# Performance work log

Measured on AMD Instinct MI355X. Metric: run time of the kernel, lower is better.

## Reference

```python
import jax, jax.numpy as jnp
import numpy as np

N = 500
HG = 16
D = 512
STEPS = 16


def _gcn_norm(edge_index, n):
    # PyG GCNConv: add self-loops, symmetric normalization
    src = jnp.concatenate([edge_index[0], jnp.arange(n)])
    dst = jnp.concatenate([edge_index[1], jnp.arange(n)])
    deg = jax.ops.segment_sum(jnp.ones_like(dst, dtype=jnp.float32), dst, num_segments=n)
    dinv = jnp.where(deg > 0, jax.lax.rsqrt(jnp.maximum(deg, 1.0)), 0.0)
    norm = dinv[src] * dinv[dst]
    return src, dst, norm


def _gcn(h, src, dst, norm, W, b):
    # h: (B, N, F) -> (B, N, HG);  out_i = sum_{j->i} norm_ji * (h_j W) + b
    hW = h @ W                              # (B, N, HG)
    t = jnp.swapaxes(hW, 0, 1)              # (N, B, HG)
    msg = t[src] * norm[:, None, None]      # (E', B, HG)
    agg = jax.ops.segment_sum(msg, dst, num_segments=h.shape[1])
    return jnp.swapaxes(agg, 0, 1) + b


def _gru_step(h, xt, Wih, Whh, bih, bhh):
    gi = xt @ Wih.T + bih                    # (B, 3D)
    gh = h @ Whh.T + bhh
    ir, iz, inn = jnp.split(gi, 3, axis=-1)
    hr, hz, hn = jnp.split(gh, 3, axis=-1)
    r = jax.nn.sigmoid(ir + hr)
    z = jax.nn.sigmoid(iz + hz)
    n = jnp.tanh(inn + r * hn)
    return (1.0 - z) * n + z * h


def setup_inputs() -> dict:
    key = jax.random.key(0)
    ks = jax.random.split(key, 16)
    B, T, F = 32, 64, 8
    E = 16000
    s = lambda fan_in: 1.0 / np.sqrt(fan_in)
    u = lambda k, shape, sc: jax.random.uniform(k, shape, jnp.float32, -sc, sc)
    return {
        "x": jax.random.normal(ks[0], (B, T, N, F), jnp.float32),
        "decoder_initial_input": jax.random.normal(ks[1], (B, N, 1), jnp.float32),
        "edge_index": jax.random.randint(ks[2], (2, E), 0, N),
        "gcn_enc_W": u(ks[3], (F, HG), s(F)),
        "gcn_enc_b": jnp.zeros((HG,), jnp.float32),
        "gcn_dec_W": u(ks[4], (1, HG), 1.0),
        "gcn_dec_b": jnp.zeros((HG,), jnp.float32),
        "enc_Wih": u(ks[5], (3 * D, N * HG), s(D)),
        "enc_Whh": u(ks[6], (3 * D, D), s(D)),
        "enc_bih": u(ks[7], (3 * D,), s(D)),
        "enc_bhh": u(ks[8], (3 * D,), s(D)),
        "dec_Wih": u(ks[9], (3 * D, N * HG), s(D)),
        "dec_Whh": u(ks[10], (3 * D, D), s(D)),
        "dec_bih": u(ks[11], (3 * D,), s(D)),
        "dec_bhh": u(ks[12], (3 * D,), s(D)),
        "fc_W": u(ks[13], (N, D), s(D)),
        "fc_b": u(ks[14], (N,), s(D)),
    }


def reference(x, decoder_initial_input, edge_index,
              gcn_enc_W, gcn_enc_b, gcn_dec_W, gcn_dec_b,
              enc_Wih, enc_Whh, enc_bih, enc_bhh,
              dec_Wih, dec_Whh, dec_bih, dec_bhh,
              fc_W, fc_b):
    B, T, n, F = x.shape
    src, dst, norm = _gcn_norm(edge_index, n)

    # ---- encoder: GCN over all (B,T) at once, then GRU scan over T ----
    emb = jax.nn.relu(_gcn(x.reshape(B * T, n, F), src, dst, norm, gcn_enc_W, gcn_enc_b))
    flat = emb.reshape(B, T, n * HG)
    xs = jnp.swapaxes(flat, 0, 1)            # (T, B, N*HG)
    h0 = jnp.zeros((B, D), jnp.float32)

    def enc_body(h, xt):
        return _gru_step(h, xt, enc_Wih, enc_Whh, enc_bih, enc_bhh), None

    hidden, _ = jax.lax.scan(enc_body, h0, xs)

    def dec_body(carry, _):
        h, inp = carry                        # inp: (B, N, 1)
        e = jax.nn.relu(_gcn(inp, src, dst, norm, gcn_dec_W, gcn_dec_b))
        h = _gru_step(h, e.reshape(B, n * HG), dec_Wih, dec_Whh, dec_bih, dec_bhh)
        out = h @ fc_W.T + fc_b               # (B, N)
        return (h, out[:, :, None]), out

    (_, _), outs = jax.lax.scan(dec_body, (hidden, decoder_initial_input), None, length=STEPS)
    return jnp.swapaxes(outs, 0, 1)           # (B, STEPS, N)
```

## Files before the change

### kernel.cpp

```cpp
#include <hip/hip_runtime.h>
#include <stdint.h>

typedef short short8 __attribute__((ext_vector_type(8)));
typedef float f32x4 __attribute__((ext_vector_type(4)));
typedef float f32x16 __attribute__((ext_vector_type(16)));

#define N_NODES 500
#define HGC 16
#define DH 512
#define T_STEPS 64
#define NB 32
#define F_IN 8
#define DSTEPS 16
#define E_EDGES 16000
#define E_TOT 16500
#define NH 8000
#define G3 1536
#define BT 2048
#define DKC 10
#define DNT 48
#define DBLK 480

__device__ __forceinline__ unsigned short f2bf(float x) {
  unsigned int u = __float_as_uint(x);
  u = (u + 0x7fffu + ((u >> 16) & 1u)) >> 16;
  return (unsigned short)u;
}

__device__ __forceinline__ void gl_lds16(const void* g, void* l) {
  __builtin_amdgcn_global_load_lds((const __attribute__((address_space(1))) void*)g,
                                   (__attribute__((address_space(3))) void*)l, 16, 0, 0);
}

__device__ __forceinline__ float sigm(float x) { return 1.f / (1.f + __expf(-x)); }

__global__ __launch_bounds__(512) void k_graph(const int* __restrict__ ei,
                                               int* __restrict__ rowptr,
                                               int* __restrict__ colg, float* __restrict__ nrmg) {
  __shared__ int degL[512];
  __shared__ int scanL[512];
  __shared__ int curL[512];
  __shared__ float dinvL[512];
  int t = threadIdx.x;
  degL[t] = (t < N_NODES) ? 1 : 0;
  __syncthreads();
  for (int e = t; e < E_EDGES; e += 512) atomicAdd(&degL[ei[E_EDGES + e]], 1);
  __syncthreads();
  int v = degL[t];
  scanL[t] = v;
  __syncthreads();
  for (int off = 1; off < 512; off <<= 1) {
    int add = (t >= off) ? scanL[t - off] : 0;
    __syncthreads();
    scanL[t] += add;
    __syncthreads();
  }
  int excl = scanL[t] - v;
  if (t < N_NODES) {
    rowptr[t] = excl;
    curL[t] = excl;
    dinvL[t] = rsqrtf((float)v);
  }
  if (t == 0) rowptr[N_NODES] = scanL[511];
  __syncthreads();
  for (int e = t; e < E_TOT; e += 512) {
    int s_, d_;
    if (e < E_EDGES) { s_ = ei[e]; d_ = ei[E_EDGES + e]; }
    else { s_ = d_ = e - E_EDGES; }
    int pos = atomicAdd(&curL[d_], 1);
    colg[pos] = s_;
    nrmg[pos] = dinvL[s_] * dinvL[d_];
  }
}

__global__ void k_f2bf_all(const float* __restrict__ a, unsigned short* __restrict__ da, int n4a,
                           const float* __restrict__ b, unsigned short* __restrict__ db, int n4b,
                           const float* __restrict__ c, unsigned short* __restrict__ dc, int n4c) {
  int i = blockIdx.x * blockDim.x + threadIdx.x;
  const float* s;
  unsigned short* d;
  int j = i;
  if (j < n4a) { s = a; d = da; }
  else {
    j -= n4a;
    if (j < n4b) { s = b; d = db; }
    else {
      j -= n4b;
      if (j >= n4c) return;
      s = c; d = dc;
    }
  }
  float4 v = ((const float4*)s)[j];
  ushort4 o;
  o.x = f2bf(v.x); o.y = f2bf(v.y); o.z = f2bf(v.z); o.w = f2bf(v.w);
  ((ushort4*)d)[j] = o;
}

__global__ void k_f2bf_fc(const float* __restrict__ fcW, unsigned short* __restrict__ fcWb) {
  int i = blockIdx.x * 256 + threadIdx.x;
  if (i >= 512 * 512 / 4) return;
  int row = i >> 7;
  ushort4 o = {0, 0, 0, 0};
  if (row < N_NODES) {
    float4 v = ((const float4*)fcW)[i];
    o.x = f2bf(v.x); o.y = f2bf(v.y); o.z = f2bf(v.z); o.w = f2bf(v.w);
  }
  ((ushort4*)fcWb)[i] = o;
}

__global__ __launch_bounds__(256) void k_repack(const float* __restrict__ dWih,
                                                unsigned short* __restrict__ wihDp) {
  int i = blockIdx.x * 256 + threadIdx.x;
  if (i >= DBLK * 50 * 32) return;
  int blob = i / 1600, r = i - blob * 1600;
  int nd = r >> 5, col = r & 31;
  int ntile = blob / DKC, kc = blob - ntile * DKC;
  const float* src = dWih + (size_t)(ntile * 32 + col) * NH + kc * 800 + nd * 16;
  short8 lo, hi;
#pragma unroll
  for (int c = 0; c < 8; ++c) {
    lo[c] = (short)f2bf(src[c]);
    hi[c] = (short)f2bf(src[c + 8]);
  }
  unsigned short* dst = wihDp + (size_t)blob * 25600 + nd * 512 + col * 8;
  *(short8*)dst = lo;
  *(short8*)(dst + 256) = hi;
}

__global__ __launch_bounds__(256) void k_transpose(const float* __restrict__ x,
                                                   unsigned short* __restrict__ xT2) {
  __shared__ float xs[N_NODES * 9];
  int g = blockIdx.x, t = threadIdx.x;
  const float4* xg = (const float4*)(x + (size_t)g * (N_NODES * F_IN));
  for (int i = t; i < N_NODES * 2; i += 256) {
    float4 v = xg[i];
    int n = i >> 1, fh = (i & 1) * 4;
    float* d = &xs[n * 9 + fh];
    d[0] = v.x; d[1] = v.y; d[2] = v.z; d[3] = v.w;
  }
  __syncthreads();
  int f = t >> 5, u = t & 31;
  short8 lo, hi;
#pragma unroll
  for (int j = 0; j < 8; ++j) {
    int n0 = u * 16 + j, n1 = n0 + 8;
    lo[j] = (short)((n0 < N_NODES) ? f2bf(xs[n0 * 9 + f]) : 0);
    hi[j] = (short)((n1 < N_NODES) ? f2bf(xs[n1 * 9 + f]) : 0);
  }
  unsigned short* dst = xT2 + (size_t)(g * 8 + f) * 512 + u * 16;
  *(short8*)dst = lo;
  *(short8*)(dst + 8) = hi;
}

__global__ __launch_bounds__(256) void k_densify(const int* __restrict__ rowptr,
                                                 const int* __restrict__ col,
                                                 const float* __restrict__ nrm,
                                                 unsigned short* __restrict__ AhatD) {
  __shared__ float row[512];
  int n = blockIdx.x, t = threadIdx.x;
  row[t] = 0.f; row[t + 256] = 0.f;
  __syncthreads();
  if (n < N_NODES) {
    int e1 = rowptr[n + 1];
    for (int e = rowptr[n] + t; e < e1; e += 256) atomicAdd(&row[col[e]], nrm[e]);
  }
  __syncthreads();
  AhatD[n * 512 + t] = f2bf(row[t]);
  AhatD[n * 512 + t + 256] = f2bf(row[t + 256]);
}

__global__ __launch_bounds__(256) void k_gemm_agg(const unsigned short* __restrict__ A,
                                                  const unsigned short* __restrict__ B,
                                                  const float* __restrict__ W,
                                                  const float* __restrict__ bias,
                                                  unsigned short* __restrict__ emb) {
  __shared__ float smem[64 * 129];
  __shared__ float Wsm[F_IN * HGC];
  __shared__ float bsm[HGC];
  unsigned short* As = (unsigned short*)smem;
  unsigned short* Bs = As + 4096;
  int t = threadIdx.x;
  if (t < F_IN * HGC) Wsm[t] = W[t];
  if (t < HGC) bsm[t] = bias[t];
  int m0 = blockIdx.x * 128, n0 = blockIdx.y * 128;
  int wave = t >> 6, lane = t & 63;
  int mh = (wave >> 1) * 64, nh = (wave & 1) * 64;
  int lrow = t >> 2, lslot = t & 3;
  f32x4 acc[4][4];
#pragma unroll
  for (int a = 0; a < 4; ++a)
#pragma unroll
    for (int b = 0; b < 4; ++b) acc[a][b] = (f32x4){0.f, 0.f, 0.f, 0.f};
  const unsigned short* ga0 = A + (size_t)(m0 + lrow) * 512 + lslot * 8;
  const unsigned short* ga1 = A + (size_t)(m0 + 64 + lrow) * 512 + lslot * 8;
  const unsigned short* gb0 = B + (size_t)(n0 + lrow) * 512 + lslot * 8;
  const unsigned short* gb1 = B + (size_t)(n0 + 64 + lrow) * 512 + lslot * 8;
  int rl = lane & 15, ks = lane >> 4;
  for (int kt = 0; kt < 16; ++kt) {
    int k0 = kt * 32;
    gl_lds16(ga0 + k0, &As[t * 8]);
    gl_lds16(ga1 + k0, &As[2048 + t * 8]);
    gl_lds16(gb0 + k0, &Bs[t * 8]);
    gl_lds16(gb1 + k0, &Bs[2048 + t * 8]);
    __syncthreads();
    short8 af[4], bfr[4];
#pragma unroll
    for (int mf = 0; mf < 4; ++mf) af[mf] = *(const short8*)&As[(mh + mf * 16 + rl) * 32 + ks * 8];
#pragma unroll
    for (int nf = 0; nf < 4; ++nf) bfr[nf] = *(const short8*)&Bs[(nh + nf * 16 + rl) * 32 + ks * 8];
#pragma unroll
    for (int mf = 0; mf < 4; ++mf)
#pragma unroll
      for (int nf = 0; nf < 4; ++nf)
        acc[mf][nf] = __builtin_amdgcn_mfma_f32_16x16x32_bf16(af[mf], bfr[nf], acc[mf][nf], 0, 0, 0);
    __syncthreads();
  }
  int rg = lane >> 4;
  for (int p = 0; p < 2; ++p) {
    if ((wave >> 1) == p) {
#pragma unroll
      for (int mf = 0; mf < 4; ++mf)
#pragma unroll
        for (int nf = 0; nf < 4; ++nf)
#pragma unroll
          for (int q = 0; q < 4; ++q)
            smem[(mf * 16 + rg * 4 + q) * 129 + nh + nf * 16 + rl] = acc[mf][nf][q];
    }
    __syncthreads();
    int gl = t >> 5, sub = t & 31;
    int g = blockIdx.x * 16 + p * 8 + gl;
#pragma unroll
    for (int j = 0; j < 4; ++j) {
      int nl = sub + 32 * j, ng = n0 + nl;
      if (ng < N_NODES) {
        float v[8];
#pragma unroll
        for (int f = 0; f < 8; ++f) v[f] = smem[(gl * 8 + f) * 129 + nl];
        short8 o0, o1;
#pragma unroll
        for (int c = 0; c < 8; ++c) {
          float s0 = bsm[c], s1 = bsm[c + 8];
#pragma unroll
          for (int f = 0; f < 8; ++f) {
            s0 += v[f] * Wsm[f * 16 + c];
            s1 += v[f] * Wsm[f * 16 + c + 8];
          }
          o0[c] = (short)f2bf(fmaxf(s0, 0.f));
          o1[c] = (short)f2bf(fmaxf(s1, 0.f));
        }
        unsigned short* dst = emb + (size_t)g * NH + ng * 16;
        *(short8*)dst = o0;
        *(short8*)(dst + 8) = o1;
      }
    }
    __syncthreads();
  }
}

__global__ __launch_bounds__(256) void k_gemm_enc(
    const unsigned short* __restrict__ A, const unsigned short* __restrict__ Bm,
    float* __restrict__ giP2) {
  __shared__ unsigned short As[128 * 32];
  __shared__ unsigned short Bs[64 * 32];
  int t = threadIdx.x;
  int m0 = blockIdx.x * 128, n0 = blockIdx.y * 64;
  int wave = t >> 6, lane = t & 63;
  int mh = (wave >> 1) * 64, nh = (wave & 1) * 32;
  int lrow = t >> 2, lslot = t & 3;
  f32x4 acc[4][2];
#pragma unroll
  for (int a = 0; a < 4; ++a)
#pragma unroll
    for (int b = 0; b < 2; ++b) acc[a][b] = (f32x4){0.f, 0.f, 0.f, 0.f};
  const unsigned short* ga0 = A + (size_t)(m0 + lrow) * NH + lslot * 8;
  const unsigned short* ga1 = A + (size_t)(m0 + 64 + lrow) * NH + lslot * 8;
  const unsigned short* gb0 = Bm + (size_t)(n0 + lrow) * NH + lslot * 8;
  int rl = lane & 15, ks = lane >> 4;
  for (int kt = 0; kt < 250; ++kt) {
    int k0 = kt * 32;
    gl_lds16(ga0 + k0, &As[t * 8]);
    gl_lds16(ga1 + k0, &As[2048 + t * 8]);
    gl_lds16(gb0 + k0, &Bs[t * 8]);
    __syncthreads();
    short8 af[4], bfr[2];
#pragma unroll
    for (int mf = 0; mf < 4; ++mf) af[mf] = *(const short8*)&As[(mh + mf * 16 + rl) * 32 + ks * 8];
#pragma unroll
    for (int nf = 0; nf < 2; ++nf) bfr[nf] = *(const short8*)&Bs[(nh + nf * 16 + rl) * 32 + ks * 8];
#pragma unroll
    for (int mf = 0; mf < 4; ++mf)
#pragma unroll
      for (int nf = 0; nf < 2; ++nf)
        acc[mf][nf] = __builtin_amdgcn_mfma_f32_16x16x32_bf16(af[mf], bfr[nf], acc[mf][nf], 0, 0, 0);
    __syncthreads();
  }
  int rg = lane >> 4;
  int gate = n0 >> 9;
#pragma unroll
  for (int mf = 0; mf < 4; ++mf)
#pragma unroll
    for (int nf = 0; nf < 2; ++nf) {
      int n = n0 + nh + nf * 16 + rl;
      int d = n & 511, blk = d >> 5, cc = d & 31;
#pragma unroll
      for (int q = 0; q < 4; ++q) {
        int m = m0 + mh + mf * 16 + rg * 4 + q;
        int s = m & 63, bb = m >> 6;
        giP2[(size_t)(s * 16 + blk) * 3072 + gate * 1024 + bb * 32 + cc] = acc[mf][nf][q];
      }
    }
}

__device__ __forceinline__ void stage_hb(const unsigned short* __restrict__ src,
                                         unsigned short* hb, int t) {
  int bw = t >> 3, i8 = t & 7;
  short8 v[8];
#pragma unroll
  for (int i = 0; i < 8; ++i)
    v[i] = *(const short8*)((const char*)src + bw * 1024 + i8 * 128 + i * 16);
#pragma unroll
  for (int i = 0; i < 8; ++i) {
    int kb = i8 * 128 + i * 16;
    *(short8*)((char*)hb + bw * 1024 + (kb ^ ((bw & 15) << 4))) = v[i];
  }
}

__device__ __forceinline__ void gru_core_g(const unsigned short* __restrict__ whhB,
                                           const unsigned short* hb, float* gh,
                                           int t, int c0) {
  int lane = t & 63, g = t >> 6;
  int b31 = lane & 31, kg = lane >> 5;
  if (g < 3) {
    f32x16 acc;
#pragma unroll
    for (int q = 0; q < 16; ++q) acc[q] = 0.f;
    const unsigned short* brow = whhB + (size_t)(g * 512 + c0 + b31) * 512 + kg * 8;
    int asw = (b31 & 15) << 4;
#pragma unroll 4
    for (int kk = 0; kk < 32; ++kk) {
      int kb = (kk * 32 + kg * 16) ^ asw;
      short8 a = *(const short8*)((const char*)hb + b31 * 1024 + kb);
      short8 b = *(const short8*)(brow + kk * 16);
      acc = __builtin_amdgcn_mfma_f32_32x32x16_bf16(a, b, acc, 0, 0, 0);
    }
#pragma unroll
    for (int q = 0; q < 16; ++q) {
      int br = (q & 3) + 8 * (q >> 2) + 4 * kg;
      gh[g * 1024 + br * 32 + b31] = acc[q];
    }
  }
}

__device__ __forceinline__ void gru_gates(const float* gi, const float* gh,
                                          const float* __restrict__ bih,
                                          const float* __restrict__ bhh,
                                          float* __restrict__ hF,
                                          unsigned short* __restrict__ hb_out,
                                          int t, int c0) {
  for (int i = t; i < 1024; i += 256) {
    int b = i >> 5, cc = i & 31, d = c0 + cc;
    float gr = gi[i] + bih[d];
    float gz = gi[1024 + i] + bih[512 + d];
    float gn = gi[2048 + i] + bih[1024 + d];
    float hr = gh[b * 32 + cc] + bhh[d];
    float hz = gh[1024 + b * 32 + cc] + bhh[512 + d];
    float hn = gh[2048 + b * 32 + cc] + bhh[1024 + d];
    float r = sigm(gr + hr), z = sigm(gz + hz);
    float nn = tanhf(gn + r * hn);
    float hp = hF[b * 512 + d];
    float hnew = (1.f - z) * nn + z * hp;
    hF[b * 512 + d] = hnew;
    hb_out[b * 512 + d] = f2bf(hnew);
  }
}

__global__ __launch_bounds__(256, 1) void k_enc_scan(
    const unsigned short* __restrict__ whhB, const float* __restrict__ giP2,
    const float* __restrict__ bih, const float* __restrict__ bhh,
    float* __restrict__ hF, unsigned short* __restrict__ hbA,
    unsigned short* __restrict__ hbB, int* __restrict__ arr) {
  __shared__ unsigned short hb[32 * 512];
  __shared__ float gh[3 * 1024];
  __shared__ float h32[1024];
  __shared__ float gi_lds[3072];
  int t = threadIdx.x, bid = blockIdx.x;
  int c0 = bid * 32;
  int lane = t & 63, g = t >> 6;
  int b31 = lane & 31, kg = lane >> 5;

  short8 wreg[32];
  if (g < 3) {
    const unsigned short* brow = whhB + (size_t)(g * 512 + c0 + b31) * 512 + kg * 8;
#pragma unroll
    for (int kk = 0; kk < 32; ++kk) wreg[kk] = *(const short8*)(brow + kk * 16);
  }
  for (int i = t; i < 1024; i += 256) h32[i] = 0.f;
  int cc = t & 31, d = c0 + cc;
  float bi_r = bih[d], bi_z = bih[512 + d], bi_n = bih[1024 + d];
  float bh_r = bhh[d], bh_z = bhh[512 + d], bh_n = bhh[1024 + d];
  int asw = (b31 & 15) << 4;
  {
    const float* src0 = giP2 + (size_t)bid * 3072;
#pragma unroll
    for (int i = 0; i < 3; ++i)
      gl_lds16(src0 + i * 1024 + t * 4, &gi_lds[i * 1024 + t * 4]);
  }
  __syncthreads();

  for (int s = 0; s < T_STEPS; ++s) {
    const unsigned short* hbin = (s & 1) ? hbB : hbA;
    unsigned short* hbout = (s & 1) ? hbA : hbB;
    if (s > 0 && t < 64) {
      for (;;) {
        int v = __hip_atomic_load(&arr[t & 15], __ATOMIC_ACQUIRE, __HIP_MEMORY_SCOPE_AGENT);
        if (__all(v >= s)) break;
        __builtin_amdgcn_s_sleep(1);
      }
    }
    __syncthreads();
    stage_hb(hbin, hb, t);
    __syncthreads();
    if (g < 3) {
      f32x16 acc0, acc1;
#pragma unroll
      for (int q = 0; q < 16; ++q) { acc0[q] = 0.f; acc1[q] = 0.f; }
      const char* abase = (const char*)hb + b31 * 1024;
#pragma unroll
      for (int kk = 0; kk < 32; ++kk) {
        int kb = (kk * 32 + kg * 16) ^ asw;
        short8 a = *(const short8*)(abase + kb);
        if (kk & 1) acc1 = __builtin_amdgcn_mfma_f32_32x32x16_bf16(a, wreg[kk], acc1, 0, 0, 0);
        else acc0 = __builtin_amdgcn_mfma_f32_32x32x16_bf16(a, wreg[kk], acc0, 0, 0, 0);
      }
#pragma unroll
      for (int q = 0; q < 16; ++q) {
        int br = (q & 3) + 8 * (q >> 2) + 4 * kg;
        gh[g * 1024 + br * 32 + b31] = acc0[q] + acc1[q];
      }
    }
    __syncthreads();
#pragma unroll
    for (int j = 0; j < 4; ++j) {
      int i = t + 256 * j;
      int b = (t >> 5) + 8 * j;
      float r = sigm(gi_lds[i] + bi_r + gh[i] + bh_r);
      float z = sigm(gi_lds[1024 + i] + bi_z + gh[1024 + i] + bh_z);
      float nn = tanhf(gi_lds[2048 + i] + bi_n + r * (gh[2048 + i] + bh_n));
      float hnew = (1.f - z) * nn + z * h32[i];
      h32[i] = hnew;
      hbout[b * 512 + d] = f2bf(hnew);
    }
    __syncthreads();
    if (g == 3 && s + 1 < T_STEPS) {
      const float* srcn = giP2 + (size_t)((s + 1) * 16 + bid) * 3072;
#pragma unroll
      for (int i = 0; i < 12; ++i)
        gl_lds16(srcn + (i * 64 + lane) * 4, &gi_lds[(i * 64 + lane) * 4]);
    }
    if (t == 0) {
      __threadfence();
      __hip_atomic_store(&arr[bid], s + 1, __ATOMIC_RELEASE, __HIP_MEMORY_SCOPE_AGENT);
    }
  }
#pragma unroll
  for (int j = 0; j < 4; ++j) {
    int i = t + 256 * j;
    int b = (t >> 5) + 8 * j;
    hF[b * 512 + d] = h32[i];
  }
}

__global__ __launch_bounds__(64) void k_dec_gemm(
    const unsigned short* __restrict__ wihDp, const unsigned short* __restrict__ E8,
    float* __restrict__ parts) {
  __shared__ unsigned short wlds[25600];
  int bid = blockIdx.x, t = threadIdx.x;
  int b31 = t & 31, kg = t >> 5;
  int ntile = bid / DKC, kc = bid - ntile * DKC;
  const unsigned short* src = wihDp + (size_t)bid * 25600;
#pragma unroll 10
  for (int i = 0; i < 50; ++i)
    gl_lds16(src + i * 512 + t * 8, (char*)wlds + i * 1024 + t * 16);
  __syncthreads();
  f32x16 acc0, acc1;
#pragma unroll
  for (int q = 0; q < 16; ++q) { acc0[q] = 0.f; acc1[q] = 0.f; }
  const unsigned short* ea = E8 + (size_t)b31 * NH + kc * 800 + kg * 8;
  const char* wb = (const char*)wlds + kg * 512 + b31 * 16;
#pragma unroll 5
  for (int nd = 0; nd < 50; nd += 2) {
    short8 a0 = *(const short8*)(ea + nd * 16);
    short8 b0 = *(const short8*)(wb + (size_t)nd * 1024);
    short8 a1 = *(const short8*)(ea + (nd + 1) * 16);
    short8 b1 = *(const short8*)(wb + (size_t)(nd + 1) * 1024);
    acc0 = __builtin_amdgcn_mfma_f32_32x32x16_bf16(a0, b0, acc0, 0, 0, 0);
    acc1 = __builtin_amdgcn_mfma_f32_32x32x16_bf16(a1, b1, acc1, 0, 0, 0);
  }
  float* pp = parts + (size_t)(kc * DNT + ntile) * 1024 + b31;
#pragma unroll
  for (int q = 0; q < 16; ++q) {
    int br = (q & 3) + 8 * (q >> 2) + 4 * kg;
    pp[br * 32] = acc0[q] + acc1[q];
  }
}

__global__ __launch_bounds__(256, 1) void k_gru_fc(
    const unsigned short* __restrict__ whhB, const float* __restrict__ parts,
    const float* __restrict__ bih, const float* __restrict__ bhh,
    float* __restrict__ hF, const unsigned short* __restrict__ hb_in,
    unsigned short* __restrict__ hb_out,
    const unsigned short* __restrict__ fcWb, const float* __restrict__ fcb,
    const float* __restrict__ Wd, const float* __restrict__ bd,
    const int* __restrict__ rowptr, const int* __restrict__ colA, const float* __restrict__ nrmA,
    float* __restrict__ out, unsigned short* __restrict__ E8,
    int* __restrict__ fGRU, int s) {
  __shared__ unsigned short hb[32 * 512];
  __shared__ float gh[3 * 1024];
  __shared__ float gi[3 * 1024];
  int t = threadIdx.x, bid = blockIdx.x;
  int c0 = bid * 32;
  int lane = t & 63, g = t >> 6;
  int b31 = lane & 31, kg = lane >> 5;
  stage_hb(hb_in, hb, t);
  for (int i = t; i < 3072; i += 256) {
    int gg = i >> 10, r = i & 1023, bb = r >> 5, cc2 = r & 31;
    float a = 0.f;
#pragma unroll
    for (int kc = 0; kc < DKC; ++kc)
      a += parts[((size_t)kc * DNT + gg * 16 + bid) * 1024 + bb * 32 + cc2];
    gi[i] = a;
  }
  __syncthreads();
  gru_core_g(whhB, hb, gh, t, c0);
  __syncthreads();
  gru_gates(gi, gh, bih, bhh, hF, hb_out, t, c0);
  __syncthreads();
  if (t == 0) {
    __threadfence();
    __hip_atomic_store(&fGRU[bid], 2 * s + 1, __ATOMIC_RELEASE, __HIP_MEMORY_SCOPE_AGENT);
  }
  if (t < 64) {
    for (;;) {
      int f = __hip_atomic_load(&fGRU[t & 15], __ATOMIC_ACQUIRE, __HIP_MEMORY_SCOPE_AGENT);
      if (__all(f >= 2 * s + 1)) break;
      __builtin_amdgcn_s_sleep(1);
    }
  }
  __syncthreads();
  stage_hb(hb_out, hb, t);
  __syncthreads();
  if (g == 0) {
    f32x16 acc;
#pragma unroll
    for (int q = 0; q < 16; ++q) acc[q] = 0.f;
    int n0 = bid * 32;
    int nrow = n0 + b31;
    const unsigned short* brow = fcWb + (size_t)nrow * 512 + kg * 8;
    const char* abase = (const char*)hb + b31 * 1024;
    int asw = (b31 & 15) << 4;
#pragma unroll 4
    for (int kk = 0; kk < 32; ++kk) {
      int kb = (kk * 32 + kg * 16) ^ asw;
      short8 a = *(const short8*)(abase + kb);
      short8 b = *(const short8*)(brow + kk * 16);
      acc = __builtin_amdgcn_mfma_f32_32x32x16_bf16(a, b, acc, 0, 0, 0);
    }
    if (nrow < N_NODES) {
      float fb = fcb[nrow];
#pragma unroll
      for (int q = 0; q < 16; ++q) {
        int br = (q & 3) + 8 * (q >> 2) + 4 * kg;
        out[(size_t)br * (DSTEPS * N_NODES) + s * N_NODES + nrow] = acc[q] + fb;
      }
    }
  }
  __syncthreads();
  if (t == 0) {
    __threadfence();
    __hip_atomic_store(&fGRU[bid], 2 * s + 2, __ATOMIC_RELEASE, __HIP_MEMORY_SCOPE_AGENT);
  }
  if (t < 64) {
    for (;;) {
      int f = __hip_atomic_load(&fGRU[t & 15], __ATOMIC_ACQUIRE, __HIP_MEMORY_SCOPE_AGENT);
      if (__all(f >= 2 * s + 2)) break;
      __builtin_amdgcn_s_sleep(1);
    }
  }
  __syncthreads();
  float* orow = gi;
  float* wds = gh;
  float* bds = gh + 16;
  int b0 = bid * 2;
  for (int i = t; i < 1000; i += 256) {
    int bb = (i >= 500) ? 1 : 0;
    int n = i - bb * 500;
    orow[bb * 512 + n] = out[(size_t)(b0 + bb) * (DSTEPS * N_NODES) + s * N_NODES + n];
  }
  if (t < HGC) { wds[t] = Wd[t]; bds[t] = bd[t]; }
  __syncthreads();
  for (int n = t; n < N_NODES; n += 256) {
    int e1 = rowptr[n + 1];
    float a0 = 0.f, a1 = 0.f;
    for (int e = rowptr[n]; e < e1; ++e) {
      int c = colA[e];
      float wv = nrmA[e];
      a0 += wv * orow[c];
      a1 += wv * orow[512 + c];
    }
    short8 l0, h0v, l1, h1v;
#pragma unroll
    for (int c = 0; c < 8; ++c) {
      l0[c] = (short)f2bf(fmaxf(a0 * wds[c] + bds[c], 0.f));
      h0v[c] = (short)f2bf(fmaxf(a0 * wds[c + 8] + bds[c + 8], 0.f));
      l1[c] = (short)f2bf(fmaxf(a1 * wds[c] + bds[c], 0.f));
      h1v[c] = (short)f2bf(fmaxf(a1 * wds[c + 8] + bds[c + 8], 0.f));
    }
    unsigned short* d0 = E8 + (size_t)b0 * NH + n * 16;
    unsigned short* d1 = E8 + (size_t)(b0 + 1) * NH + n * 16;
    *(short8*)d0 = l0;
    *(short8*)(d0 + 8) = h0v;
    *(short8*)d1 = l1;
    *(short8*)(d1 + 8) = h1v;
  }
}

__global__ __launch_bounds__(256) void k_agg0(
    const float* __restrict__ dec0, const float* __restrict__ Wd, const float* __restrict__ bd,
    const int* __restrict__ rowptr, const int* __restrict__ col, const float* __restrict__ nrm,
    unsigned short* __restrict__ E8) {
  __shared__ float irow[N_NODES];
  __shared__ float wds[HGC], bds[HGC];
  int b = blockIdx.x, t = threadIdx.x;
  for (int n = t; n < N_NODES; n += 256) irow[n] = dec0[b * N_NODES + n];
  if (t < HGC) { wds[t] = Wd[t]; bds[t] = bd[t]; }
  __syncthreads();
  for (int n = t; n < N_NODES; n += 256) {
    int e1 = rowptr[n + 1];
    float a = 0.f;
    for (int e = rowptr[n]; e < e1; ++e) a += nrm[e] * irow[col[e]];
    short8 lo, hi;
#pragma unroll
    for (int c = 0; c < 8; ++c) {
      lo[c] = (short)f2bf(fmaxf(a * wds[c] + bds[c], 0.f));
      hi[c] = (short)f2bf(fmaxf(a * wds[c + 8] + bds[c + 8], 0.f));
    }
    unsigned short* dst = E8 + (size_t)b * NH + n * 16;
    *(short8*)dst = lo;
    *(short8*)(dst + 8) = hi;
  }
}

extern "C" void kernel_launch(void* const* d_in, const int* in_sizes, int n_in,
                              void* d_out, int out_size, void* d_ws, size_t ws_size,
                              hipStream_t stream) {
  const float* x = (const float*)d_in[0];
  const float* dec0 = (const float*)d_in[1];
  const int* ei = (const int*)d_in[2];
  const float* gWe = (const float*)d_in[3];
  const float* gbe = (const float*)d_in[4];
  const float* gWd = (const float*)d_in[5];
  const float* gbd = (const float*)d_in[6];
  const float* eWih = (const float*)d_in[7];
  const float* eWhh = (const float*)d_in[8];
  const float* ebih = (const float*)d_in[9];
  const float* ebhh = (const float*)d_in[10];
  const float* dWih = (const float*)d_in[11];
  const float* dWhh = (const float*)d_in[12];
  const float* dbih = (const float*)d_in[13];
  const float* dbhh = (const float*)d_in[14];
  const float* fcW = (const float*)d_in[15];
  const float* fcb = (const float*)d_in[16];
  float* out = (float*)d_out;
  (void)in_sizes; (void)n_in; (void)out_size; (void)ws_size;

  char* w = (char*)d_ws;
  size_t off = 0;
  auto alloc = [&](size_t bytes) -> void* {
    void* p = w + off;
    off = (off + bytes + 255) & ~(size_t)255;
    return p;
  };
  int* rowptr = (int*)alloc(512 * 4);
  int* colA = (int*)alloc(E_TOT * 4);
  float* nrmA = (float*)alloc(E_TOT * 4);
  unsigned short* whhE = (unsigned short*)alloc((size_t)G3 * DH * 2);
  unsigned short* whhD = (unsigned short*)alloc((size_t)G3 * DH * 2);
  unsigned short* AhatD = (unsigned short*)alloc(512 * 512 * 2);
  unsigned short* fcWb = (unsigned short*)alloc(512 * 512 * 2);
  float* hF = (float*)alloc(NB * DH * 4);
  unsigned short* hbX = (unsigned short*)alloc(NB * DH * 2);
  int* arr = (int*)alloc(256);
  int* fGRU = (int*)alloc(256);
  unsigned short* hbY = (unsigned short*)alloc(NB * DH * 2);
  unsigned short* E8 = (unsigned short*)alloc((size_t)NB * NH * 2);
  unsigned short* emb = (unsigned short*)alloc((size_t)BT * NH * 2);
  char* wihE_parts = (char*)alloc((size_t)G3 * NH * 2);
  unsigned short* wihE = (unsigned short*)wihE_parts;
  float* parts = (float*)wihE_parts;
  unsigned short* wihDp = (unsigned short*)alloc((size_t)DBLK * 25600 * 2);
  char* xT2_giP = (char*)alloc((size_t)16384 * 512 * 2);
  unsigned short* xT2 = (unsigned short*)xT2_giP;
  float* giP2 = (float*)xT2_giP;

  hipMemsetAsync(hF, 0, NB * DH * 4 + NB * DH * 2 + 256 + 256, stream);

  k_graph<<<1, 512, 0, stream>>>(ei, rowptr, colA, nrmA);

  int n4w = G3 * NH / 4;
  int n4h = G3 * DH / 4;
  k_f2bf_all<<<(n4w + 2 * n4h + 255) / 256, 256, 0, stream>>>(
      eWih, wihE, n4w, eWhh, whhE, n4h, dWhh, whhD, n4h);
  k_f2bf_fc<<<256, 256, 0, stream>>>(fcW, fcWb);
  k_repack<<<3000, 256, 0, stream>>>(dWih, wihDp);

  k_transpose<<<BT, 256, 0, stream>>>(x, xT2);
  k_densify<<<512, 256, 0, stream>>>(rowptr, colA, nrmA, AhatD);
  k_gemm_agg<<<dim3(128, 4), 256, 0, stream>>>(xT2, AhatD, gWe, gbe, emb);

  k_gemm_enc<<<dim3(BT / 128, G3 / 64), 256, 0, stream>>>(emb, wihE, giP2);

  k_enc_scan<<<16, 256, 0, stream>>>(whhE, giP2, ebih, ebhh, hF, hbX, hbY, arr);

  k_agg0<<<NB, 256, 0, stream>>>(dec0, gWd, gbd, rowptr, colA, nrmA, E8);

  for (int s = 0; s < DSTEPS; ++s) {
    const unsigned short* hbin = (s & 1) ? hbY : hbX;
    unsigned short* hbout = (s & 1) ? hbX : hbY;
    k_dec_gemm<<<DBLK, 64, 0, stream>>>(wihDp, E8, parts);
    k_gru_fc<<<16, 256, 0, stream>>>(whhD, parts, dbih, dbhh, hF, hbin, hbout,
                                     fcWb, fcb, gWd, gbd, rowptr, colA, nrmA,
                                     out, E8, fGRU, s);
  }
}
```

Baseline: 1.482 ms.

## Run encoder GRU scan on 8 blocks of 512 threads with row-major gate inputs

The persistent encoder scan now uses 8 blocks of 512 threads, each owning 64 hidden columns with six waves covering three gates times two halves. Fewer blocks means fewer participants in the cross-block flag barrier each step. The input-gate GEMM now writes a plain row-major output, and gate inputs are read straight from global memory into registers instead of being prefetched into LDS. The hidden state stays in registers, and the fc-weight conversion is merged into the shared bf16 conversion kernel to save one launch. The trade-off is half as many CUs on the serial scan, and a single MFMA accumulator chain per wave instead of two interleaved ones.

```diff
diff --git a/kernel.cpp b/kernel.cpp
--- a/kernel.cpp
+++ b/kernel.cpp
@@ -75,7 +75,8 @@
 
 __global__ void k_f2bf_all(const float* __restrict__ a, unsigned short* __restrict__ da, int n4a,
                            const float* __restrict__ b, unsigned short* __restrict__ db, int n4b,
-                           const float* __restrict__ c, unsigned short* __restrict__ dc, int n4c) {
+                           const float* __restrict__ c, unsigned short* __restrict__ dc, int n4c,
+                           const float* __restrict__ f, unsigned short* __restrict__ df) {
   int i = blockIdx.x * blockDim.x + threadIdx.x;
   const float* s;
   unsigned short* d;
@@ -86,26 +87,25 @@
     if (j < n4b) { s = b; d = db; }
     else {
       j -= n4b;
-      if (j >= n4c) return;
-      s = c; d = dc;
+      if (j < n4c) { s = c; d = dc; }
+      else {
+        j -= n4c;
+        if (j >= 512 * 128) return;
+        int row = j >> 7;
+        ushort4 o = {0, 0, 0, 0};
+        if (row < N_NODES) {
+          float4 v = ((const float4*)f)[j];
+          o.x = f2bf(v.x); o.y = f2bf(v.y); o.z = f2bf(v.z); o.w = f2bf(v.w);
+        }
+        ((ushort4*)df)[j] = o;
+        return;
+      }
     }
   }
   float4 v = ((const float4*)s)[j];
   ushort4 o;
   o.x = f2bf(v.x); o.y = f2bf(v.y); o.z = f2bf(v.z); o.w = f2bf(v.w);
   ((ushort4*)d)[j] = o;
-}
-
-__global__ void k_f2bf_fc(const float* __restrict__ fcW, unsigned short* __restrict__ fcWb) {
-  int i = blockIdx.x * 256 + threadIdx.x;
-  if (i >= 512 * 512 / 4) return;
-  int row = i >> 7;
-  ushort4 o = {0, 0, 0, 0};
-  if (row < N_NODES) {
-    float4 v = ((const float4*)fcW)[i];
-    o.x = f2bf(v.x); o.y = f2bf(v.y); o.z = f2bf(v.z); o.w = f2bf(v.w);
-  }
-  ((ushort4*)fcWb)[i] = o;
 }
 
 __global__ __launch_bounds__(256) void k_repack(const float* __restrict__ dWih,
@@ -259,7 +259,7 @@
 
 __global__ __launch_bounds__(256) void k_gemm_enc(
     const unsigned short* __restrict__ A, const unsigned short* __restrict__ Bm,
-    float* __restrict__ giP2) {
+    float* __restrict__ C) {
   __shared__ unsigned short As[128 * 32];
   __shared__ unsigned short Bs[64 * 32];
   int t = threadIdx.x;
@@ -295,19 +295,14 @@
     __syncthreads();
   }
   int rg = lane >> 4;
-  int gate = n0 >> 9;
 #pragma unroll
   for (int mf = 0; mf < 4; ++mf)
 #pragma unroll
     for (int nf = 0; nf < 2; ++nf) {
+      int m = m0 + mh + mf * 16 + rg * 4;
       int n = n0 + nh + nf * 16 + rl;
-      int d = n & 511, blk = d >> 5, cc = d & 31;
-#pragma unroll
-      for (int q = 0; q < 4; ++q) {
-        int m = m0 + mh + mf * 16 + rg * 4 + q;
-        int s = m & 63, bb = m >> 6;
-        giP2[(size_t)(s * 16 + blk) * 3072 + gate * 1024 + bb * 32 + cc] = acc[mf][nf][q];
-      }
+#pragma unroll
+      for (int q = 0; q < 4; ++q) C[(size_t)(m + q) * G3 + n] = acc[mf][nf][q];
     }
 }
 
@@ -374,89 +369,99 @@
   }
 }
 
-__global__ __launch_bounds__(256, 1) void k_enc_scan(
-    const unsigned short* __restrict__ whhB, const float* __restrict__ giP2,
+__global__ __launch_bounds__(512, 1) void k_enc_scan(
+    const unsigned short* __restrict__ whhB, const float* __restrict__ giE,
     const float* __restrict__ bih, const float* __restrict__ bhh,
     float* __restrict__ hF, unsigned short* __restrict__ hbA,
     unsigned short* __restrict__ hbB, int* __restrict__ arr) {
   __shared__ unsigned short hb[32 * 512];
-  __shared__ float gh[3 * 1024];
-  __shared__ float h32[1024];
-  __shared__ float gi_lds[3072];
+  __shared__ float gh[6 * 1024];
   int t = threadIdx.x, bid = blockIdx.x;
-  int c0 = bid * 32;
-  int lane = t & 63, g = t >> 6;
+  int c0 = bid * 64;
+  int lane = t & 63, w = t >> 6;
   int b31 = lane & 31, kg = lane >> 5;
 
   short8 wreg[32];
-  if (g < 3) {
-    const unsigned short* brow = whhB + (size_t)(g * 512 + c0 + b31) * 512 + kg * 8;
+  if (w < 6) {
+    int gate = w >> 1, half = w & 1;
+    const unsigned short* brow =
+        whhB + (size_t)(gate * 512 + c0 + half * 32 + b31) * 512 + kg * 8;
 #pragma unroll
     for (int kk = 0; kk < 32; ++kk) wreg[kk] = *(const short8*)(brow + kk * 16);
   }
-  for (int i = t; i < 1024; i += 256) h32[i] = 0.f;
-  int cc = t & 31, d = c0 + cc;
+  int cc = t & 63, d = c0 + cc;
   float bi_r = bih[d], bi_z = bih[512 + d], bi_n = bih[1024 + d];
   float bh_r = bhh[d], bh_z = bhh[512 + d], bh_n = bhh[1024 + d];
+  int hf = cc >> 5, c31 = cc & 31;
+  float h32r[4];
+#pragma unroll
+  for (int j = 0; j < 4; ++j) h32r[j] = 0.f;
   int asw = (b31 & 15) << 4;
-  {
-    const float* src0 = giP2 + (size_t)bid * 3072;
-#pragma unroll
-    for (int i = 0; i < 3; ++i)
-      gl_lds16(src0 + i * 1024 + t * 4, &gi_lds[i * 1024 + t * 4]);
-  }
   __syncthreads();
 
   for (int s = 0; s < T_STEPS; ++s) {
     const unsigned short* hbin = (s & 1) ? hbB : hbA;
     unsigned short* hbout = (s & 1) ? hbA : hbB;
+    float gr_r[4], gz_r[4], gn_r[4];
+#pragma unroll
+    for (int j = 0; j < 4; ++j) {
+      int b = (t >> 6) + 8 * j;
+      const float* gp = giE + (size_t)(b * T_STEPS + s) * G3 + d;
+      gr_r[j] = gp[0]; gz_r[j] = gp[512]; gn_r[j] = gp[1024];
+    }
     if (s > 0 && t < 64) {
       for (;;) {
-        int v = __hip_atomic_load(&arr[t & 15], __ATOMIC_ACQUIRE, __HIP_MEMORY_SCOPE_AGENT);
+        int v = __hip_atomic_load(&arr[t & 7], __ATOMIC_ACQUIRE, __HIP_MEMORY_SCOPE_AGENT);
         if (__all(v >= s)) break;
         __builtin_amdgcn_s_sleep(1);
       }
     }
     __syncthreads();
-    stage_hb(hbin, hb, t);
-    __syncthreads();
-    if (g < 3) {
-      f32x16 acc0, acc1;
-#pragma unroll
-      for (int q = 0; q < 16; ++q) { acc0[q] = 0.f; acc1[q] = 0.f; }
+    {
+      int bw = t >> 4, i8 = t & 15;
+      short8 v[4];
+#pragma unroll
+      for (int i = 0; i < 4; ++i)
+        v[i] = *(const short8*)((const char*)hbin + bw * 1024 + i8 * 64 + i * 16);
+#pragma unroll
+      for (int i = 0; i < 4; ++i) {
+        int kb = i8 * 64 + i * 16;
+        *(short8*)((char*)hb + bw * 1024 + (kb ^ ((bw & 15) << 4))) = v[i];
+      }
+    }
+    __syncthreads();
+    if (w < 6) {
+      f32x16 acc;
+#pragma unroll
+      for (int q = 0; q < 16; ++q) acc[q] = 0.f;
       const char* abase = (const char*)hb + b31 * 1024;
-#pragma unroll
+#pragma unroll 4
       for (int kk = 0; kk < 32; ++kk) {
         int kb = (kk * 32 + kg * 16) ^ asw;
         short8 a = *(const short8*)(abase + kb);
-        if (kk & 1) acc1 = __builtin_amdgcn_mfma_f32_32x32x16_bf16(a, wreg[kk], acc1, 0, 0, 0);
-        else acc0 = __builtin_amdgcn_mfma_f32_32x32x16_bf16(a, wreg[kk], acc0, 0, 0, 0);
+        acc = __builtin_amdgcn_mfma_f32_32x32x16_bf16(a, wreg[kk], acc, 0, 0, 0);
       }
 #pragma unroll
       for (int q = 0; q < 16; ++q) {
         int br = (q & 3) + 8 * (q >> 2) + 4 * kg;
-        gh[g * 1024 + br * 32 + b31] = acc0[q] + acc1[q];
+        gh[w * 1024 + br * 32 + b31] = acc[q];
       }
     }
     __syncthreads();
 #pragma unroll
     for (int j = 0; j < 4; ++j) {
-      int i = t + 256 * j;
-      int b = (t >> 5) + 8 * j;
-      float r = sigm(gi_lds[i] + bi_r + gh[i] + bh_r);
-      float z = sigm(gi_lds[1024 + i] + bi_z + gh[1024 + i] + bh_z);
-      float nn = tanhf(gi_lds[2048 + i] + bi_n + r * (gh[2048 + i] + bh_n));
-      float hnew = (1.f - z) * nn + z * h32[i];
-      h32[i] = hnew;
+      int b = (t >> 6) + 8 * j;
+      float ghr = gh[(0 * 2 + hf) * 1024 + b * 32 + c31];
+      float ghz = gh[(1 * 2 + hf) * 1024 + b * 32 + c31];
+      float ghn = gh[(2 * 2 + hf) * 1024 + b * 32 + c31];
+      float r = sigm(gr_r[j] + bi_r + ghr + bh_r);
+      float z = sigm(gz_r[j] + bi_z + ghz + bh_z);
+      float nn = tanhf(gn_r[j] + bi_n + r * (ghn + bh_n));
+      float hnew = (1.f - z) * nn + z * h32r[j];
+      h32r[j] = hnew;
       hbout[b * 512 + d] = f2bf(hnew);
     }
     __syncthreads();
-    if (g == 3 && s + 1 < T_STEPS) {
-      const float* srcn = giP2 + (size_t)((s + 1) * 16 + bid) * 3072;
-#pragma unroll
-      for (int i = 0; i < 12; ++i)
-        gl_lds16(srcn + (i * 64 + lane) * 4, &gi_lds[(i * 64 + lane) * 4]);
-    }
     if (t == 0) {
       __threadfence();
       __hip_atomic_store(&arr[bid], s + 1, __ATOMIC_RELEASE, __HIP_MEMORY_SCOPE_AGENT);
@@ -464,9 +469,8 @@
   }
 #pragma unroll
   for (int j = 0; j < 4; ++j) {
-    int i = t + 256 * j;
-    int b = (t >> 5) + 8 * j;
-    hF[b * 512 + d] = h32[i];
+    int b = (t >> 6) + 8 * j;
+    hF[b * 512 + d] = h32r[j];
   }
 }
 
@@ -553,8 +557,7 @@
     f32x16 acc;
 #pragma unroll
     for (int q = 0; q < 16; ++q) acc[q] = 0.f;
-    int n0 = bid * 32;
-    int nrow = n0 + b31;
+    int nrow = bid * 32 + b31;
     const unsigned short* brow = fcWb + (size_t)nrow * 512 + kg * 8;
     const char* abase = (const char*)hb + b31 * 1024;
     int asw = (b31 & 15) << 4;
@@ -698,9 +701,9 @@
   unsigned short* wihE = (unsigned short*)wihE_parts;
   float* parts = (float*)wihE_parts;
   unsigned short* wihDp = (unsigned short*)alloc((size_t)DBLK * 25600 * 2);
-  char* xT2_giP = (char*)alloc((size_t)16384 * 512 * 2);
-  unsigned short* xT2 = (unsigned short*)xT2_giP;
-  float* giP2 = (float*)xT2_giP;
+  char* xT2_giE = (char*)alloc((size_t)16384 * 512 * 2);
+  unsigned short* xT2 = (unsigned short*)xT2_giE;
+  float* giE = (float*)xT2_giE;
 
   hipMemsetAsync(hF, 0, NB * DH * 4 + NB * DH * 2 + 256 + 256, stream);
 
@@ -708,18 +711,17 @@
 
   int n4w = G3 * NH / 4;
   int n4h = G3 * DH / 4;
-  k_f2bf_all<<<(n4w + 2 * n4h + 255) / 256, 256, 0, stream>>>(
-      eWih, wihE, n4w, eWhh, whhE, n4h, dWhh, whhD, n4h);
-  k_f2bf_fc<<<256, 256, 0, stream>>>(fcW, fcWb);
+  k_f2bf_all<<<(n4w + 2 * n4h + 512 * 128 + 255) / 256, 256, 0, stream>>>(
+      eWih, wihE, n4w, eWhh, whhE, n4h, dWhh, whhD, n4h, fcW, fcWb);
   k_repack<<<3000, 256, 0, stream>>>(dWih, wihDp);
 
   k_transpose<<<BT, 256, 0, stream>>>(x, xT2);
   k_densify<<<512, 256, 0, stream>>>(rowptr, colA, nrmA, AhatD);
   k_gemm_agg<<<dim3(128, 4), 256, 0, stream>>>(xT2, AhatD, gWe, gbe, emb);
 
-  k_gemm_enc<<<dim3(BT / 128, G3 / 64), 256, 0, stream>>>(emb, wihE, giP2);
-
-  k_enc_scan<<<16, 256, 0, stream>>>(whhE, giP2, ebih, ebhh, hF, hbX, hbY, arr);
+  k_gemm_enc<<<dim3(BT / 128, G3 / 64), 256, 0, stream>>>(emb, wihE, giE);
+
+  k_enc_scan<<<8, 512, 0, stream>>>(whhE, giE, ebih, ebhh, hF, hbX, hbY, arr);
 
   k_agg0<<<NB, 256, 0, stream>>>(dec0, gWd, gbd, rowptr, colA, nrmA, E8);
 
```

Result: slower. 1.689 ms (+14.0%).
